# Kernel optimization log

Measured on AMD Instinct MI355X. Metric: run time of the kernel, lower is better.

## Reference

```python
import jax, jax.numpy as jnp
import numpy as np


def setup_inputs() -> dict:
    key = jax.random.key(0)
    k1, k2 = jax.random.split(key)
    STATE_LEN, SEQ_LEN, D = 8192, 8192, 1024
    user_emb = jax.random.normal(k1, (STATE_LEN, D), dtype=jnp.float32)
    id_emb = jax.random.normal(k2, (SEQ_LEN, D), dtype=jnp.float32)
    return {"user_emb": user_emb, "id_emb": id_emb}


def reference(user_emb, id_emb):
    # attn_energies[i, j] = user_emb[i] . id_emb[j]  -> single GEMM
    energies = jnp.einsum('id,jd->ij', user_emb, id_emb)  # [state_len, seq_len]
    # F.softmax on 2D tensor defaults to dim=1 (rows)
    return jax.nn.softmax(energies, axis=-1)
```

## Files before the change

kernel.cpp:

```cpp
#include <hip/hip_runtime.h>
#include <hip/hip_bf16.h>
#include <stdint.h>

typedef __attribute__((ext_vector_type(8))) short bf16x8;
typedef __attribute__((ext_vector_type(4))) float f32x4;

typedef const __attribute__((address_space(1))) void* gas_ptr;
typedef __attribute__((address_space(3))) void* lds_ptr_t;

__device__ __forceinline__ unsigned short f32_to_bf16_rtn(float x) {
    unsigned u = __float_as_uint(x);
    u += 0x7FFFu + ((u >> 16) & 1u);
    return (unsigned short)(u >> 16);
}
__device__ __forceinline__ float bf16_bits_to_f32(unsigned short h) {
    return __uint_as_float(((unsigned)h) << 16);
}

__global__ __launch_bounds__(256) void split_hi_lo(
    const float* __restrict__ A, const float* __restrict__ B,
    unsigned short* __restrict__ Ahi, unsigned short* __restrict__ Alo,
    unsigned short* __restrict__ Bhi, unsigned short* __restrict__ Blo, int n4)
{
    int i = blockIdx.x * 256 + threadIdx.x;
    if (i >= n4) return;
    float4 a = ((const float4*)A)[i];
    float4 b = ((const float4*)B)[i];
    ushort4 h, l;

    h.x = f32_to_bf16_rtn(a.x); l.x = f32_to_bf16_rtn(a.x - bf16_bits_to_f32(h.x));
    h.y = f32_to_bf16_rtn(a.y); l.y = f32_to_bf16_rtn(a.y - bf16_bits_to_f32(h.y));
    h.z = f32_to_bf16_rtn(a.z); l.z = f32_to_bf16_rtn(a.z - bf16_bits_to_f32(h.z));
    h.w = f32_to_bf16_rtn(a.w); l.w = f32_to_bf16_rtn(a.w - bf16_bits_to_f32(h.w));
    ((ushort4*)Ahi)[i] = h; ((ushort4*)Alo)[i] = l;

    h.x = f32_to_bf16_rtn(b.x); l.x = f32_to_bf16_rtn(b.x - bf16_bits_to_f32(h.x));
    h.y = f32_to_bf16_rtn(b.y); l.y = f32_to_bf16_rtn(b.y - bf16_bits_to_f32(h.y));
    h.z = f32_to_bf16_rtn(b.z); l.z = f32_to_bf16_rtn(b.z - bf16_bits_to_f32(h.z));
    h.w = f32_to_bf16_rtn(b.w); l.w = f32_to_bf16_rtn(b.w - bf16_bits_to_f32(h.w));
    ((ushort4*)Bhi)[i] = h; ((ushort4*)Blo)[i] = l;
}

__device__ __forceinline__ void wait_vm8_bar()
{
    asm volatile("s_waitcnt vmcnt(8)" ::: "memory");
    __builtin_amdgcn_s_barrier();
    asm volatile("" ::: "memory");
}
__device__ __forceinline__ void wait_vm0_bar()
{
    asm volatile("s_waitcnt vmcnt(0)" ::: "memory");
    __builtin_amdgcn_s_barrier();
    asm volatile("" ::: "memory");
}
__device__ __forceinline__ void bar_only()
{
    asm volatile("" ::: "memory");
    __builtin_amdgcn_s_barrier();
    asm volatile("" ::: "memory");
}

template<int KC, int NC>
__global__ __launch_bounds__(256) void gemm_presplit(
    const __hip_bfloat16* __restrict__ Ahi, const __hip_bfloat16* __restrict__ Alo,
    const __hip_bfloat16* __restrict__ Bhi, const __hip_bfloat16* __restrict__ Blo,
    float* __restrict__ out, int M, int N, int K)
{
    const int Kd = (KC > 0) ? KC : K;
    const int Nd = (NC > 0) ? NC : N;

    __shared__ char sm[65536];
    const int tid  = threadIdx.x;
    const int lane = tid & 63;
    const int w    = tid >> 6;
    const int bm = blockIdx.y, bn = blockIdx.x;
    const int wm = (w >> 1) * 64;
    const int wn = (w & 1) * 64;

    f32x4 acc[4][4] = {};

    const int sfetch = (tid & 3) ^ ((tid >> 3) & 3);
    const size_t offA = (size_t)(bm * 128 + (tid >> 2)) * Kd + sfetch * 8;
    const size_t offB = (size_t)(bn * 128 + (tid >> 2)) * Kd + sfetch * 8;
    const __hip_bfloat16* pAh = Ahi + offA;
    const __hip_bfloat16* pAl = Alo + offA;
    const __hip_bfloat16* pBh = Bhi + offB;
    const __hip_bfloat16* pBl = Blo + offB;
    const size_t half = (size_t)64 * Kd;
    char* dst0 = sm + tid * 16;

    const int rA = lane & 15;
    const int ca = (lane >> 4) ^ ((lane >> 1) & 3);
    const char* aP = sm +         (wm + rA) * 64 + ca * 16;
    const char* bP = sm + 16384 + (wn + rA) * 64 + ca * 16;

#define STAGE(BO, kk) do { \
    __builtin_amdgcn_global_load_lds((gas_ptr)(pAh + (kk)),        (lds_ptr_t)(dst0 + (BO)),          16, 0, 0); \
    __builtin_amdgcn_global_load_lds((gas_ptr)(pAh + half + (kk)), (lds_ptr_t)(dst0 + (BO) + 4096),   16, 0, 0); \
    __builtin_amdgcn_global_load_lds((gas_ptr)(pAl + (kk)),        (lds_ptr_t)(dst0 + (BO) + 8192),   16, 0, 0); \
    __builtin_amdgcn_global_load_lds((gas_ptr)(pAl + half + (kk)), (lds_ptr_t)(dst0 + (BO) + 12288),  16, 0, 0); \
    __builtin_amdgcn_global_load_lds((gas_ptr)(pBh + (kk)),        (lds_ptr_t)(dst0 + (BO) + 16384),  16, 0, 0); \
    __builtin_amdgcn_global_load_lds((gas_ptr)(pBh + half + (kk)), (lds_ptr_t)(dst0 + (BO) + 20480),  16, 0, 0); \
    __builtin_amdgcn_global_load_lds((gas_ptr)(pBl + (kk)),        (lds_ptr_t)(dst0 + (BO) + 24576),  16, 0, 0); \
    __builtin_amdgcn_global_load_lds((gas_ptr)(pBl + half + (kk)), (lds_ptr_t)(dst0 + (BO) + 28672),  16, 0, 0); \
} while (0)

#define COMPUTE(BO) do { \
    bf16x8 bh[4], bl[4]; \
    _Pragma("unroll") \
    for (int j = 0; j < 4; ++j) { \
        bh[j] = *(const bf16x8*)(bP + (BO) + j * 1024); \
        bl[j] = *(const bf16x8*)(bP + (BO) + j * 1024 + 8192); \
    } \
    __builtin_amdgcn_s_setprio(1); \
    _Pragma("unroll") \
    for (int i = 0; i < 4; ++i) { \
        bf16x8 ah = *(const bf16x8*)(aP + (BO) + i * 1024); \
        bf16x8 al = *(const bf16x8*)(aP + (BO) + i * 1024 + 8192); \
        _Pragma("unroll") \
        for (int j = 0; j < 4; ++j) { \
            acc[i][j] = __builtin_amdgcn_mfma_f32_16x16x32_bf16(ah, bh[j], acc[i][j], 0, 0, 0); \
            acc[i][j] = __builtin_amdgcn_mfma_f32_16x16x32_bf16(al, bh[j], acc[i][j], 0, 0, 0); \
            acc[i][j] = __builtin_amdgcn_mfma_f32_16x16x32_bf16(ah, bl[j], acc[i][j], 0, 0, 0); \
        } \
    } \
    __builtin_amdgcn_s_setprio(0); \
} while (0)

    STAGE(0, 0);
#pragma unroll 2
    for (int k0 = 0; k0 < Kd - 64; k0 += 64) {
        STAGE(32768, k0 + 32);
        wait_vm8_bar();
        COMPUTE(0);
        bar_only();
        STAGE(0, k0 + 64);
        wait_vm8_bar();
        COMPUTE(32768);
        bar_only();
    }
    STAGE(32768, Kd - 32);
    wait_vm8_bar();
    COMPUTE(0);
    bar_only();
    wait_vm0_bar();
    COMPUTE(32768);

#undef STAGE
#undef COMPUTE

    const int r0 = bm * 128 + wm + ((lane >> 4) << 2);
    const int c0 = bn * 128 + wn + rA;
#pragma unroll
    for (int i = 0; i < 4; ++i)
#pragma unroll
        for (int j = 0; j < 4; ++j)
#pragma unroll
            for (int r = 0; r < 4; ++r)
                __builtin_nontemporal_store(
                    acc[i][j][r],
                    &out[(size_t)(r0 + i * 16 + r) * Nd + (c0 + j * 16)]);
}

__global__ __launch_bounds__(256) void gemm_fallback(
    const float* __restrict__ Af, const float* __restrict__ Bf,
    float* __restrict__ out, int M, int N, int K)
{
    __shared__ char sm[32768];
    const int tid  = threadIdx.x;
    const int lane = tid & 63;
    const int w    = tid >> 6;
    const int bm = blockIdx.y, bn = blockIdx.x;
    const int wm = (w >> 1) * 64;
    const int wn = (w & 1) * 64;

    f32x4 acc[4][4] = {};
    const int sfetch = (tid & 3) ^ ((tid >> 3) & 3);
    const int rA = lane & 15;
    const int ca = (lane >> 4) ^ ((lane >> 1) & 3);
    const char* aP = sm +         (wm + rA) * 64 + ca * 16;
    const char* bP = sm + 16384 + (wn + rA) * 64 + ca * 16;

    for (int k0 = 0; k0 < K; k0 += 32) {
        __syncthreads();
#pragma unroll
        for (int c = 0; c < 4; ++c) {
            const bool isA = (c < 2);
            const int row = ((c & 1) << 6) + (tid >> 2);
            const float* src = (isA ? Af + (size_t)(bm * 128 + row) * K
                                    : Bf + (size_t)(bn * 128 + row) * K)
                               + k0 + ((tid & 3) << 3);
            f32x4 v0 = *(const f32x4*)src;
            f32x4 v1 = *(const f32x4*)(src + 4);
            float vv[8] = {v0.x, v0.y, v0.z, v0.w, v1.x, v1.y, v1.z, v1.w};
            bf16x8 h, l;
#pragma unroll
            for (int j = 0; j < 8; ++j) {
                unsigned short hb = f32_to_bf16_rtn(vv[j]);
                unsigned short lb = f32_to_bf16_rtn(vv[j] - bf16_bits_to_f32(hb));
                h[j] = (short)hb; l[j] = (short)lb;
            }
            const int g = row * 64 + sfetch * 16;
            *(bf16x8*)(sm + (isA ? 0 : 16384) + g) = h;
            *(bf16x8*)(sm + (isA ? 8192 : 24576) + g) = l;
        }
        __syncthreads();

        bf16x8 bh[4], bl[4];
#pragma unroll
        for (int j = 0; j < 4; ++j) {
            bh[j] = *(const bf16x8*)(bP + j * 1024);
            bl[j] = *(const bf16x8*)(bP + j * 1024 + 8192);
        }
#pragma unroll
        for (int i = 0; i < 4; ++i) {
            bf16x8 ah = *(const bf16x8*)(aP + i * 1024);
            bf16x8 al = *(const bf16x8*)(aP + i * 1024 + 8192);
#pragma unroll
            for (int j = 0; j < 4; ++j) {
                acc[i][j] = __builtin_amdgcn_mfma_f32_16x16x32_bf16(ah, bh[j], acc[i][j], 0, 0, 0);
                acc[i][j] = __builtin_amdgcn_mfma_f32_16x16x32_bf16(al, bh[j], acc[i][j], 0, 0, 0);
                acc[i][j] = __builtin_amdgcn_mfma_f32_16x16x32_bf16(ah, bl[j], acc[i][j], 0, 0, 0);
            }
        }
    }

    const int r0 = bm * 128 + wm + ((lane >> 4) << 2);
    const int c0 = bn * 128 + wn + rA;
#pragma unroll
    for (int i = 0; i < 4; ++i)
#pragma unroll
        for (int j = 0; j < 4; ++j)
#pragma unroll
            for (int r = 0; r < 4; ++r)
                __builtin_nontemporal_store(
                    acc[i][j][r],
                    &out[(size_t)(r0 + i * 16 + r) * N + (c0 + j * 16)]);
}

__device__ __forceinline__ void lgkm_barrier()
{
    asm volatile("s_waitcnt lgkmcnt(0)" ::: "memory");
    __builtin_amdgcn_s_barrier();
    asm volatile("" ::: "memory");
}

__device__ __forceinline__ void softmax_row(
    f32x4 (&v)[8], f32x4 (&vn)[8], const f32x4* __restrict__ pn, bool pref,
    f32x4* __restrict__ pout, int tid, int slot,
    float (*smax)[4], float (*ssum)[4])
{
    if (pref) {
#pragma unroll
        for (int i = 0; i < 8; ++i) vn[i] = pn[tid + (i << 8)];
    }
    float m = -3.402823466e+38f;
#pragma unroll
    for (int i = 0; i < 8; ++i)
        m = fmaxf(m, fmaxf(fmaxf(v[i].x, v[i].y), fmaxf(v[i].z, v[i].w)));
#pragma unroll
    for (int o = 32; o >= 1; o >>= 1) m = fmaxf(m, __shfl_xor(m, o));
    if ((tid & 63) == 0) smax[slot][tid >> 6] = m;
    lgkm_barrier();
    m = fmaxf(fmaxf(smax[slot][0], smax[slot][1]), fmaxf(smax[slot][2], smax[slot][3]));

    float s = 0.f;
#pragma unroll
    for (int i = 0; i < 8; ++i) {
        v[i].x = __expf(v[i].x - m);
        v[i].y = __expf(v[i].y - m);
        v[i].z = __expf(v[i].z - m);
        v[i].w = __expf(v[i].w - m);
        s += (v[i].x + v[i].y) + (v[i].z + v[i].w);
    }
#pragma unroll
    for (int o = 32; o >= 1; o >>= 1) s += __shfl_xor(s, o);
    if ((tid & 63) == 0) ssum[slot][tid >> 6] = s;
    lgkm_barrier();
    s = (ssum[slot][0] + ssum[slot][1]) + (ssum[slot][2] + ssum[slot][3]);
    const float r = 1.0f / s;
#pragma unroll
    for (int i = 0; i < 8; ++i) {
        v[i] *= r;
        __builtin_nontemporal_store(v[i], &pout[tid + (i << 8)]);
    }
}

__global__ __launch_bounds__(256) void softmax_rows_8192(float* __restrict__ d)
{
    const int tid = threadIdx.x;
    __shared__ float smax[2][4], ssum[2][4];

    f32x4* p0 = (f32x4*)(d + (size_t)blockIdx.x * 4 * 8192);
    f32x4 va[8], vb[8];
#pragma unroll
    for (int i = 0; i < 8; ++i) va[i] = p0[tid + (i << 8)];

    softmax_row(va, vb, p0 + 2048, true,  p0,        tid, 0, smax, ssum);
    softmax_row(vb, va, p0 + 4096, true,  p0 + 2048, tid, 1, smax, ssum);
    softmax_row(va, vb, p0 + 6144, true,  p0 + 4096, tid, 0, smax, ssum);
    softmax_row(vb, va, p0,        false, p0 + 6144, tid, 1, smax, ssum);
}

extern "C" void kernel_launch(void* const* d_in, const int* in_sizes, int n_in,
                              void* d_out, int out_size, void* d_ws, size_t ws_size,
                              hipStream_t stream)
{
    const float* A = (const float*)d_in[0];
    const float* B = (const float*)d_in[1];
    float* out = (float*)d_out;
    const int K = 1024;
    const int M = in_sizes[0] / K;
    const int N = in_sizes[1] / K;
    const size_t elemsA = (size_t)M * K;
    const size_t elemsB = (size_t)N * K;
    const size_t need = 2 * (elemsA + elemsB) * sizeof(unsigned short);

    dim3 grid(N / 128, M / 128);
    const bool presplit = (ws_size >= need) && (M == N) && (K % 64 == 0) && (K >= 128);

    if (presplit) {
        unsigned short* Ahi = (unsigned short*)d_ws;
        unsigned short* Alo = Ahi + elemsA;
        unsigned short* Bhi = Alo + elemsA;
        unsigned short* Blo = Bhi + elemsB;
        const int n4 = (int)(elemsA / 4);
        split_hi_lo<<<(n4 + 255) / 256, 256, 0, stream>>>(A, B, Ahi, Alo, Bhi, Blo, n4);
        if (K == 1024 && N == 8192) {
            gemm_presplit<1024, 8192><<<grid, 256, 0, stream>>>(
                (const __hip_bfloat16*)Ahi, (const __hip_bfloat16*)Alo,
                (const __hip_bfloat16*)Bhi, (const __hip_bfloat16*)Blo,
                out, M, N, K);
        } else {
            gemm_presplit<0, 0><<<grid, 256, 0, stream>>>(
                (const __hip_bfloat16*)Ahi, (const __hip_bfloat16*)Alo,
                (const __hip_bfloat16*)Bhi, (const __hip_bfloat16*)Blo,
                out, M, N, K);
        }
    } else {
        gemm_fallback<<<grid, 256, 0, stream>>>(A, B, out, M, N, K);
    }
    softmax_rows_8192<<<M / 4, 256, 0, stream>>>(out);
}
```

Baseline: 725.1 us.

## Use 256x256 block tiles with 512 threads for the presplit bf16x3 GEMM

Adds a GEMM kernel that computes 256x256 output tiles per block using 8 waves (each 128x64) and 128 KB of dynamic LDS for double buffering, and uses it for the 8192x8192x1024 shape. Larger tiles halve the global/L2 traffic per FLOP and raise the MFMA-to-LDS-read ratio per wave. In exchange, occupancy drops to one block per CU because of the LDS footprint and the larger accumulator register count. The grid shrinks to 1024 blocks, and this kernel relies on the 160 KB LDS available on MI355X. The generic 128-tile kernel is kept for other shapes.

Measured after the change: 752.3 us. 1.04x slower.

```diff
diff --git a/kernel.cpp b/kernel.cpp
--- a/kernel.cpp
+++ b/kernel.cpp
@@ -15,6 +15,25 @@
 }
 __device__ __forceinline__ float bf16_bits_to_f32(unsigned short h) {
     return __uint_as_float(((unsigned)h) << 16);
+}
+
+__device__ __forceinline__ void wait_vm8_bar()
+{
+    asm volatile("s_waitcnt vmcnt(8)" ::: "memory");
+    __builtin_amdgcn_s_barrier();
+    asm volatile("" ::: "memory");
+}
+__device__ __forceinline__ void wait_vm0_bar()
+{
+    asm volatile("s_waitcnt vmcnt(0)" ::: "memory");
+    __builtin_amdgcn_s_barrier();
+    asm volatile("" ::: "memory");
+}
+__device__ __forceinline__ void bar_only()
+{
+    asm volatile("" ::: "memory");
+    __builtin_amdgcn_s_barrier();
+    asm volatile("" ::: "memory");
 }
 
 __global__ __launch_bounds__(256) void split_hi_lo(
@@ -41,34 +60,114 @@
     ((ushort4*)Bhi)[i] = h; ((ushort4*)Blo)[i] = l;
 }
 
-__device__ __forceinline__ void wait_vm8_bar()
-{
-    asm volatile("s_waitcnt vmcnt(8)" ::: "memory");
-    __builtin_amdgcn_s_barrier();
-    asm volatile("" ::: "memory");
-}
-__device__ __forceinline__ void wait_vm0_bar()
-{
-    asm volatile("s_waitcnt vmcnt(0)" ::: "memory");
-    __builtin_amdgcn_s_barrier();
-    asm volatile("" ::: "memory");
-}
-__device__ __forceinline__ void bar_only()
-{
-    asm volatile("" ::: "memory");
-    __builtin_amdgcn_s_barrier();
-    asm volatile("" ::: "memory");
-}
-
 template<int KC, int NC>
-__global__ __launch_bounds__(256) void gemm_presplit(
+__global__ __launch_bounds__(512) void gemm_presplit256(
+    const __hip_bfloat16* __restrict__ Ahi, const __hip_bfloat16* __restrict__ Alo,
+    const __hip_bfloat16* __restrict__ Bhi, const __hip_bfloat16* __restrict__ Blo,
+    float* __restrict__ out)
+{
+    const int Kd = KC;
+    const int Nd = NC;
+    extern __shared__ char sm[];
+
+    const int tid  = threadIdx.x;
+    const int lane = tid & 63;
+    const int w    = tid >> 6;
+    const int bm = blockIdx.y, bn = blockIdx.x;
+    const int wm = (w >> 2) * 128;
+    const int wn = (w & 3) * 64;
+
+    f32x4 acc[8][4] = {};
+
+    const int sfetch = (tid & 3) ^ ((tid >> 3) & 3);
+    const size_t offA = (size_t)(bm * 256 + (tid >> 2)) * Kd + sfetch * 8;
+    const size_t offB = (size_t)(bn * 256 + (tid >> 2)) * Kd + sfetch * 8;
+    const __hip_bfloat16* pAh = Ahi + offA;
+    const __hip_bfloat16* pAl = Alo + offA;
+    const __hip_bfloat16* pBh = Bhi + offB;
+    const __hip_bfloat16* pBl = Blo + offB;
+    const size_t half = (size_t)128 * Kd;
+    char* dst0 = sm + tid * 16;
+
+    const int rA = lane & 15;
+    const int ca = (lane >> 4) ^ ((lane >> 1) & 3);
+    const char* aP = sm +         (wm >> 6) * 4096 + rA * 64 + ca * 16;
+    const char* bP = sm + 32768 + (wn >> 6) * 4096 + rA * 64 + ca * 16;
+
+#define STAGE(BO, kk) do { \
+    __builtin_amdgcn_global_load_lds((gas_ptr)(pAh + (kk)),        (lds_ptr_t)(dst0 + (BO)),          16, 0, 0); \
+    __builtin_amdgcn_global_load_lds((gas_ptr)(pAh + half + (kk)), (lds_ptr_t)(dst0 + (BO) + 8192),   16, 0, 0); \
+    __builtin_amdgcn_global_load_lds((gas_ptr)(pAl + (kk)),        (lds_ptr_t)(dst0 + (BO) + 16384),  16, 0, 0); \
+    __builtin_amdgcn_global_load_lds((gas_ptr)(pAl + half + (kk)), (lds_ptr_t)(dst0 + (BO) + 24576),  16, 0, 0); \
+    __builtin_amdgcn_global_load_lds((gas_ptr)(pBh + (kk)),        (lds_ptr_t)(dst0 + (BO) + 32768),  16, 0, 0); \
+    __builtin_amdgcn_global_load_lds((gas_ptr)(pBh + half + (kk)), (lds_ptr_t)(dst0 + (BO) + 40960),  16, 0, 0); \
+    __builtin_amdgcn_global_load_lds((gas_ptr)(pBl + (kk)),        (lds_ptr_t)(dst0 + (BO) + 49152),  16, 0, 0); \
+    __builtin_amdgcn_global_load_lds((gas_ptr)(pBl + half + (kk)), (lds_ptr_t)(dst0 + (BO) + 57344),  16, 0, 0); \
+} while (0)
+
+#define COMPUTE(BO) do { \
+    bf16x8 bh[4], bl[4]; \
+    _Pragma("unroll") \
+    for (int j = 0; j < 4; ++j) { \
+        bh[j] = *(const bf16x8*)(bP + (BO) + j * 1024); \
+        bl[j] = *(const bf16x8*)(bP + (BO) + j * 1024 + 16384); \
+    } \
+    __builtin_amdgcn_s_setprio(1); \
+    _Pragma("unroll") \
+    for (int i = 0; i < 8; ++i) { \
+        const int ao = ((i >> 2) << 12) + ((i & 3) << 10); \
+        bf16x8 ah = *(const bf16x8*)(aP + (BO) + ao); \
+        bf16x8 al = *(const bf16x8*)(aP + (BO) + ao + 16384); \
+        _Pragma("unroll") \
+        for (int j = 0; j < 4; ++j) { \
+            acc[i][j] = __builtin_amdgcn_mfma_f32_16x16x32_bf16(ah, bh[j], acc[i][j], 0, 0, 0); \
+            acc[i][j] = __builtin_amdgcn_mfma_f32_16x16x32_bf16(al, bh[j], acc[i][j], 0, 0, 0); \
+            acc[i][j] = __builtin_amdgcn_mfma_f32_16x16x32_bf16(ah, bl[j], acc[i][j], 0, 0, 0); \
+        } \
+    } \
+    __builtin_amdgcn_s_setprio(0); \
+} while (0)
+
+    STAGE(0, 0);
+#pragma unroll 2
+    for (int k0 = 0; k0 < Kd - 64; k0 += 64) {
+        STAGE(65536, k0 + 32);
+        wait_vm8_bar();
+        COMPUTE(0);
+        bar_only();
+        STAGE(0, k0 + 64);
+        wait_vm8_bar();
+        COMPUTE(65536);
+        bar_only();
+    }
+    STAGE(65536, Kd - 32);
+    wait_vm8_bar();
+    COMPUTE(0);
+    bar_only();
+    wait_vm0_bar();
+    COMPUTE(65536);
+
+#undef STAGE
+#undef COMPUTE
+
+    const int r0 = bm * 256 + wm + ((lane >> 4) << 2);
+    const int c0 = bn * 256 + wn + rA;
+#pragma unroll
+    for (int i = 0; i < 8; ++i)
+#pragma unroll
+        for (int j = 0; j < 4; ++j)
+#pragma unroll
+            for (int r = 0; r < 4; ++r)
+                __builtin_nontemporal_store(
+                    acc[i][j][r],
+                    &out[(size_t)(r0 + i * 16 + r) * Nd + (c0 + j * 16)]);
+}
+
+__global__ __launch_bounds__(256) void gemm_presplit128(
     const __hip_bfloat16* __restrict__ Ahi, const __hip_bfloat16* __restrict__ Alo,
     const __hip_bfloat16* __restrict__ Bhi, const __hip_bfloat16* __restrict__ Blo,
     float* __restrict__ out, int M, int N, int K)
 {
-    const int Kd = (KC > 0) ? KC : K;
-    const int Nd = (NC > 0) ? NC : N;
-
     __shared__ char sm[65536];
     const int tid  = threadIdx.x;
     const int lane = tid & 63;
@@ -80,13 +179,13 @@
     f32x4 acc[4][4] = {};
 
     const int sfetch = (tid & 3) ^ ((tid >> 3) & 3);
-    const size_t offA = (size_t)(bm * 128 + (tid >> 2)) * Kd + sfetch * 8;
-    const size_t offB = (size_t)(bn * 128 + (tid >> 2)) * Kd + sfetch * 8;
+    const size_t offA = (size_t)(bm * 128 + (tid >> 2)) * K + sfetch * 8;
+    const size_t offB = (size_t)(bn * 128 + (tid >> 2)) * K + sfetch * 8;
     const __hip_bfloat16* pAh = Ahi + offA;
     const __hip_bfloat16* pAl = Alo + offA;
     const __hip_bfloat16* pBh = Bhi + offB;
     const __hip_bfloat16* pBl = Blo + offB;
-    const size_t half = (size_t)64 * Kd;
+    const size_t half = (size_t)64 * K;
     char* dst0 = sm + tid * 16;
 
     const int rA = lane & 15;
@@ -128,8 +227,7 @@
 } while (0)
 
     STAGE(0, 0);
-#pragma unroll 2
-    for (int k0 = 0; k0 < Kd - 64; k0 += 64) {
+    for (int k0 = 0; k0 < K - 64; k0 += 64) {
         STAGE(32768, k0 + 32);
         wait_vm8_bar();
         COMPUTE(0);
@@ -139,7 +237,7 @@
         COMPUTE(32768);
         bar_only();
     }
-    STAGE(32768, Kd - 32);
+    STAGE(32768, K - 32);
     wait_vm8_bar();
     COMPUTE(0);
     bar_only();
@@ -159,7 +257,7 @@
             for (int r = 0; r < 4; ++r)
                 __builtin_nontemporal_store(
                     acc[i][j][r],
-                    &out[(size_t)(r0 + i * 16 + r) * Nd + (c0 + j * 16)]);
+                    &out[(size_t)(r0 + i * 16 + r) * N + (c0 + j * 16)]);
 }
 
 __global__ __launch_bounds__(256) void gemm_fallback(
@@ -316,7 +414,6 @@
     const size_t elemsB = (size_t)N * K;
     const size_t need = 2 * (elemsA + elemsB) * sizeof(unsigned short);
 
-    dim3 grid(N / 128, M / 128);
     const bool presplit = (ws_size >= need) && (M == N) && (K % 64 == 0) && (K >= 128);
 
     if (presplit) {
@@ -326,18 +423,20 @@
         unsigned short* Blo = Bhi + elemsB;
         const int n4 = (int)(elemsA / 4);
         split_hi_lo<<<(n4 + 255) / 256, 256, 0, stream>>>(A, B, Ahi, Alo, Bhi, Blo, n4);
-        if (K == 1024 && N == 8192) {
-            gemm_presplit<1024, 8192><<<grid, 256, 0, stream>>>(
+        if (M == 8192 && N == 8192 && K == 1024) {
+            dim3 grid(N / 256, M / 256);
+            gemm_presplit256<1024, 8192><<<grid, 512, 131072, stream>>>(
                 (const __hip_bfloat16*)Ahi, (const __hip_bfloat16*)Alo,
-                (const __hip_bfloat16*)Bhi, (const __hip_bfloat16*)Blo,
-                out, M, N, K);
+                (const __hip_bfloat16*)Bhi, (const __hip_bfloat16*)Blo, out);
         } else {
-            gemm_presplit<0, 0><<<grid, 256, 0, stream>>>(
+            dim3 grid(N / 128, M / 128);
+            gemm_presplit128<<<grid, 256, 0, stream>>>(
                 (const __hip_bfloat16*)Ahi, (const __hip_bfloat16*)Alo,
                 (const __hip_bfloat16*)Bhi, (const __hip_bfloat16*)Blo,
                 out, M, N, K);
         }
     } else {
+        dim3 grid(N / 128, M / 128);
         gemm_fallback<<<grid, 256, 0, stream>>>(A, B, out, M, N, K);
     }
     softmax_rows_8192<<<M / 4, 256, 0, stream>>>(out);
```
